# Kernel tuning notes

Hardware: AMD Instinct MI355X
Metric: run time of the kernel (lower is better)

## Reference

```python
import jax, jax.numpy as jnp
import numpy as np

B, W, C, N = 2, 2048, 512, 8
K = C // N                      # 64
HALF = K * (K + 1) // 2 - K     # strict upper-triangle count
EPS = 1e-5


def _layernorm(x, gamma, beta):
    mu = jnp.mean(x, axis=-1, keepdims=True)
    var = jnp.mean(jnp.square(x - mu), axis=-1, keepdims=True)
    return (x - mu) * jax.lax.rsqrt(var + EPS) * gamma + beta


def _build_metric(halves, diagonals):
    # symmetric per-head metric: strict upper triangle from `halves`,
    # mirrored, diagonal overwritten by `diagonals` (diag of m+m^T is 0).
    iu0, iu1 = np.triu_indices(K, k=1)
    m = jnp.zeros((N, K, K), dtype=halves.dtype).at[:, iu0, iu1].set(halves)
    m = m + jnp.swapaxes(m, -1, -2)
    d = np.arange(K)
    return m.at[:, d, d].set(diagonals)


def setup_inputs() -> dict:
    key = jax.random.key(0)
    ks = jax.random.split(key, 9)
    return {
        "x1": jax.random.normal(ks[0], (B, W, C), jnp.float32),
        "x2": jax.random.normal(ks[1], (B, W, C), jnp.float32),
        "gamma": jnp.ones((C,), jnp.float32),
        "beta": jnp.zeros((C,), jnp.float32),
        "proj_nck": jax.random.normal(ks[2], (N, C, K), jnp.float32) * (C ** -0.5),
        "halves": jax.random.normal(ks[3], (N, HALF), jnp.float32) * 0.05,
        "diagonals": jax.random.normal(ks[4], (N, K), jnp.float32) * 0.05,
        "W_mixer": jax.random.normal(ks[5], (C, C), jnp.float32) * 0.02,
        "b_mixer": jnp.zeros((C,), jnp.float32),
    }


def reference(x1, x2, gamma, beta, proj_nck, halves, diagonals, W_mixer, b_mixer):
    x1n = _layernorm(x1, gamma, beta)
    x2n = _layernorm(x2, gamma, beta)
    metric_nkk = _build_metric(halves, diagonals)

    # per-head projections (same projection used for both sequences)
    p1_bnwk = jnp.einsum("bwc,nck->bnwk", x1n, proj_nck)
    p2_bnwk = jnp.einsum("bwc,nck->bnwk", x2n, proj_nck)

    # bilinear metric scores  Q . M . K^T  -> [B, N, W, W]
    dots_bnww = jnp.einsum("bnwk,nkj,bnvj->bnwv", p1_bnwk, metric_nkk, p2_bnwk)

    # NOTE: the original computes a scaled/masked softmax of dots_bnww but
    # never uses it for the output; the value mix uses the RAW dot products.
    # We omit the dead softmax — output math is identical.

    nudged_bnwk = jnp.einsum("bnwv,bnvk->bnwk", dots_bnww, p1_bnwk)
    nudged_bwc = jnp.transpose(nudged_bnwk, (0, 2, 1, 3)).reshape(x1.shape[0], x1.shape[1], C)
    return nudged_bwc @ W_mixer.T + b_mixer
```

## Files before the change

### kernel.cpp

```cpp
#include <hip/hip_runtime.h>

typedef unsigned short u16;
typedef __attribute__((ext_vector_type(8))) short short8;
typedef __attribute__((ext_vector_type(4))) float f32x4;

#define HALFN 2016

__device__ __forceinline__ u16 f2b_rn(float x) {
    union { float f; unsigned u; } v; v.f = x;
    unsigned r = v.u + 0x7FFFu + ((v.u >> 16) & 1u);
    return (u16)(r >> 16);
}

__device__ __forceinline__ void gll16(const void* g, void* s) {
    __builtin_amdgcn_global_load_lds(
        (const __attribute__((address_space(1))) unsigned int*)g,
        (__attribute__((address_space(3))) unsigned int*)s, 16, 0, 0);
}

__global__ __launch_bounds__(256) void ln_prep(const float* __restrict__ x1,
                                               const float* __restrict__ x2,
                                               const float* __restrict__ gamma,
                                               const float* __restrict__ beta,
                                               const float* __restrict__ proj,
                                               u16* __restrict__ Xh,
                                               u16* __restrict__ Pwh,
                                               float* __restrict__ S) {
    __shared__ float ls[8], lq[8];
    __shared__ float tile[64][65];
    const int bid = blockIdx.x, t = threadIdx.x;

    if (bid < 8192) {
        const float* src = (bid < 4096) ? (x1 + (size_t)bid * 512)
                                        : (x2 + (size_t)(bid - 4096) * 512);
        float2 v = *(const float2*)&src[t * 2];
        float s  = v.x + v.y;
        float sq = v.x * v.x + v.y * v.y;
        #pragma unroll
        for (int off = 32; off > 0; off >>= 1) {
            s  += __shfl_down(s, off);
            sq += __shfl_down(sq, off);
        }
        int wave = t >> 6, lane = t & 63;
        if (lane == 0) { ls[wave] = s; lq[wave] = sq; }
        __syncthreads();
        if (t == 0) {
            float Sm = 0.f, Q = 0.f;
            #pragma unroll
            for (int i = 0; i < 4; i++) { Sm += ls[i]; Q += lq[i]; }
            float mu  = Sm * (1.0f / 512.0f);
            float var = Q * (1.0f / 512.0f) - mu * mu;
            ls[4] = mu;
            lq[4] = rsqrtf(var + 1e-5f);
        }
        __syncthreads();
        float mu = ls[4], rs = lq[4];
        float2 g  = *(const float2*)&gamma[t * 2];
        float2 bb = *(const float2*)&beta[t * 2];
        float o0 = (v.x - mu) * rs * g.x + bb.x;
        float o1 = (v.y - mu) * rs * g.y + bb.y;
        ushort2 H; H.x = f2b_rn(o0); H.y = f2b_rn(o1);
        *(ushort2*)&Xh[(size_t)bid * 512 + t * 2] = H;
    } else if (bid < 8256) {
        const int id = bid - 8192;
        const int n = id >> 3, c0 = (id & 7) * 64;
        #pragma unroll
        for (int i = 0; i < 4; i++) {
            int flat = i * 256 + t;
            int c = flat >> 4, k4 = (flat & 15) * 4;
            float4 v = *(const float4*)&proj[(size_t)n * 32768 + (size_t)(c0 + c) * 64 + k4];
            tile[c][k4 + 0] = v.x; tile[c][k4 + 1] = v.y;
            tile[c][k4 + 2] = v.z; tile[c][k4 + 3] = v.w;
        }
        __syncthreads();
        #pragma unroll
        for (int i = 0; i < 16; i++) {
            int flat = i * 256 + t;
            int k = flat >> 6, c = flat & 63;
            Pwh[(size_t)(n * 64 + k) * 512 + c0 + c] = f2b_rn(tile[c][k]);
        }
    } else {
        float4 z = {0.f, 0.f, 0.f, 0.f};
        #pragma unroll
        for (int i = 0; i < 64; i++)
            *(float4*)&S[(size_t)(i * 256 + t) * 4] = z;
    }
}

template<int TM, int TN>
__device__ __forceinline__ void gemm_core_a1b1(const u16* __restrict__ A,
                                               const u16* __restrict__ B,
                                               int m0, int n0, u16* lds,
                                               f32x4 (&acc)[TM / 32][TN / 32]) {
    constexpr int MI = TM / 32, NI = TN / 32;
    constexpr int LA = TM * 32;
    const int t = threadIdx.x;
    const int lane = t & 63;
    const int w = t >> 6, wm = w & 1, wn = w >> 1;
    const int fr = lane & 15, q = lane >> 4;

    int aoff[MI], boff[NI];
    #pragma unroll
    for (int i = 0; i < MI; i++) {
        int r = wm * (TM / 2) + i * 16 + fr;
        aoff[i] = r * 32 + ((q ^ ((r >> 1) & 3)) * 8);
    }
    #pragma unroll
    for (int j = 0; j < NI; j++) {
        int r = wn * (TN / 2) + j * 16 + fr;
        boff[j] = r * 32 + ((q ^ ((r >> 1) & 3)) * 8);
    }

    for (int kt = 0; kt < 512; kt += 32) {
        #pragma unroll
        for (int p = 0; p < TM / 64; p++) {
            int o = p * 4096 + t * 16;
            int r = o >> 6;
            int kc = ((o >> 4) & 3) ^ ((r >> 1) & 3);
            gll16(A + (size_t)(m0 + r) * 512 + kt + kc * 8, lds + (o >> 1));
        }
        #pragma unroll
        for (int p = 0; p < TN / 64; p++) {
            int o = p * 4096 + t * 16;
            int r = o >> 6;
            int kc = ((o >> 4) & 3) ^ ((r >> 1) & 3);
            gll16(B + (size_t)(n0 + r) * 512 + kt + kc * 8, lds + LA + (o >> 1));
        }
        __syncthreads();
        short8 af[MI], bf[NI];
        #pragma unroll
        for (int i = 0; i < MI; i++)
            af[i] = *(const short8*)(lds + aoff[i]);
        #pragma unroll
        for (int j = 0; j < NI; j++)
            bf[j] = *(const short8*)(lds + LA + boff[j]);
        #pragma unroll
        for (int i = 0; i < MI; i++)
            #pragma unroll
            for (int j = 0; j < NI; j++)
                acc[i][j] = __builtin_amdgcn_mfma_f32_16x16x32_bf16(af[i], bf[j], acc[i][j], 0, 0, 0);
        __syncthreads();
    }
}

__global__ __launch_bounds__(256) void gemm_proj_mfma(const u16* __restrict__ Xh,
                                                      const u16* __restrict__ Pwh,
                                                      u16* __restrict__ PPh,
                                                      u16* __restrict__ PPT1h,
                                                      u16* __restrict__ PPT2h) {
    __shared__ u16 lds[6144];
    f32x4 acc[4][2] = {};
    const int m0 = blockIdx.x * 128, n0 = blockIdx.y * 64;
    gemm_core_a1b1<128, 64>(Xh, Pwh, m0, n0, lds, acc);
    const int t = threadIdx.x, lane = t & 63, w = t >> 6, wm = w & 1, wn = w >> 1;
    const int fr = lane & 15, q = lane >> 4;
    const int src2 = (m0 >= 4096);
    const int b = (m0 & 4095) >> 11;
    const int v00 = m0 & 2047;
    #pragma unroll
    for (int i = 0; i < 4; i++) {
        int mloc = wm * 64 + i * 16 + q * 4;
        int v = v00 + mloc;
        #pragma unroll
        for (int j = 0; j < 2; j++) {
            int n = n0 + wn * 32 + j * 16 + fr;
            u16 hs[4];
            #pragma unroll
            for (int r = 0; r < 4; r++) hs[r] = f2b_rn(acc[i][j][r]);
            ushort4 hv; hv.x = hs[0]; hv.y = hs[1]; hv.z = hs[2]; hv.w = hs[3];
            if (!src2) {
                #pragma unroll
                for (int r = 0; r < 4; r++)
                    PPh[(size_t)(m0 + mloc + r) * 512 + n] = hs[r];
                *(ushort4*)&PPT1h[((size_t)(b * 512 + n)) * 2048 + v] = hv;
            } else {
                *(ushort4*)&PPT2h[((size_t)(b * 512 + n)) * 2048 + v] = hv;
            }
        }
    }
}

__global__ __launch_bounds__(256) void s_kernel(const u16* __restrict__ PPT2h,
                                                const u16* __restrict__ PPT1h,
                                                float* __restrict__ S) {
    __shared__ u16 lds[4096];
    const int bn = blockIdx.x, b = bn >> 3, n = bn & 7;
    const u16* A = PPT2h + ((size_t)(b * 512 + n * 64)) * 2048;
    const u16* B = PPT1h + ((size_t)(b * 512 + n * 64)) * 2048;
    const int t = threadIdx.x, lane = t & 63, w = t >> 6, wm = w & 1, wn = w >> 1;
    const int fr = lane & 15, q = lane >> 4;

    int aoff[2], boff[2];
    #pragma unroll
    for (int i = 0; i < 2; i++) {
        int r = wm * 32 + i * 16 + fr;
        aoff[i] = r * 32 + ((q ^ ((r >> 1) & 3)) * 8);
    }
    #pragma unroll
    for (int j = 0; j < 2; j++) {
        int r = wn * 32 + j * 16 + fr;
        boff[j] = r * 32 + ((q ^ ((r >> 1) & 3)) * 8);
    }
    const int o = t * 16;
    const int rr = o >> 6;
    const int kc = ((o >> 4) & 3) ^ ((rr >> 1) & 3);
    const int le = o >> 1;

    f32x4 acc[2][2] = {};
    const int k0 = blockIdx.y * 128;
    for (int kt = k0; kt < k0 + 128; kt += 32) {
        size_t g = (size_t)rr * 2048 + kt + kc * 8;
        gll16(A + g, lds + le);
        gll16(B + g, lds + 2048 + le);
        __syncthreads();
        short8 af[2], bf[2];
        #pragma unroll
        for (int i = 0; i < 2; i++) af[i] = *(const short8*)(lds + aoff[i]);
        #pragma unroll
        for (int j = 0; j < 2; j++) bf[j] = *(const short8*)(lds + 2048 + boff[j]);
        #pragma unroll
        for (int i = 0; i < 2; i++)
            #pragma unroll
            for (int j = 0; j < 2; j++)
                acc[i][j] = __builtin_amdgcn_mfma_f32_16x16x32_bf16(af[i], bf[j], acc[i][j], 0, 0, 0);
        __syncthreads();
    }
    float* Sb = S + (size_t)bn * 4096;
    #pragma unroll
    for (int i = 0; i < 2; i++) {
        int jrow = wm * 32 + i * 16 + q * 4;
        #pragma unroll
        for (int j = 0; j < 2; j++) {
            int kk = wn * 32 + j * 16 + fr;
            #pragma unroll
            for (int r = 0; r < 4; r++)
                atomicAdd(&Sb[(jrow + r) * 64 + kk], acc[i][j][r]);
        }
    }
}

__global__ __launch_bounds__(256) void tu_kernel(const float* __restrict__ S,
                                                 const float* __restrict__ halves,
                                                 const float* __restrict__ diagonals,
                                                 const float* __restrict__ Wm,
                                                 u16* __restrict__ UTh) {
    __shared__ float Ms[64][65];
    __shared__ float Gs[64][68];
    __shared__ float Ts[64][68];
    const int bid = blockIdx.x, t = threadIdx.x;
    const int bn = bid >> 3, b = bn >> 3, n = bn & 7, cy = bid & 7;

    for (int idx = t; idx < 4096; idx += 256) {
        int r = idx >> 6, c = idx & 63;
        float val;
        if (r == c) {
            val = diagonals[n * 64 + r];
        } else {
            int rr = (r < c) ? r : c;
            int cc = (r < c) ? c : r;
            int h = rr * 63 - (rr * (rr - 1)) / 2 + (cc - rr - 1);
            val = halves[n * HALFN + h];
        }
        Ms[r][c] = val;
    }
    for (int idx = t; idx < 4096; idx += 256)
        Gs[idx >> 6][idx & 63] = S[(size_t)bn * 4096 + idx];
    __syncthreads();

    {
        const int k = t & 63, lq = t >> 6;
        float a[16] = {};
        for (int j = 0; j < 64; j++) {
            float m = Ms[k][j];
            const float* gp = &Gs[j][lq * 16];
            #pragma unroll
            for (int u4 = 0; u4 < 4; u4++) {
                float4 g4 = *(const float4*)&gp[u4 * 4];
                a[u4 * 4 + 0] = fmaf(m, g4.x, a[u4 * 4 + 0]);
                a[u4 * 4 + 1] = fmaf(m, g4.y, a[u4 * 4 + 1]);
                a[u4 * 4 + 2] = fmaf(m, g4.z, a[u4 * 4 + 2]);
                a[u4 * 4 + 3] = fmaf(m, g4.w, a[u4 * 4 + 3]);
            }
        }
        int pos = (lq ^ (k & 3)) * 16;
        #pragma unroll
        for (int u4 = 0; u4 < 4; u4++) {
            float4 v4 = {a[u4 * 4 + 0], a[u4 * 4 + 1], a[u4 * 4 + 2], a[u4 * 4 + 3]};
            *(float4*)&Ts[k][pos + u4 * 4] = v4;
        }
    }
    __syncthreads();

    const int k2 = t & 63, cgp = t >> 6;
    const int c0 = cy * 64 + cgp * 16;
    float uacc[16] = {};
    #pragma unroll
    for (int kkc = 0; kkc < 4; kkc++) {
        const float* tp = &Ts[k2][(kkc ^ (k2 & 3)) * 16];
        float ts[16];
        #pragma unroll
        for (int u = 0; u < 4; u++) {
            float4 t4 = *(const float4*)&tp[u * 4];
            ts[u * 4 + 0] = t4.x; ts[u * 4 + 1] = t4.y;
            ts[u * 4 + 2] = t4.z; ts[u * 4 + 3] = t4.w;
        }
        #pragma unroll
        for (int i = 0; i < 16; i++) {
            const float* wrow = &Wm[(size_t)(c0 + i) * 512 + n * 64 + kkc * 16];
            #pragma unroll
            for (int u = 0; u < 4; u++) {
                float4 w4 = *(const float4*)&wrow[u * 4];
                uacc[i] = fmaf(ts[u * 4 + 0], w4.x, uacc[i]);
                uacc[i] = fmaf(ts[u * 4 + 1], w4.y, uacc[i]);
                uacc[i] = fmaf(ts[u * 4 + 2], w4.z, uacc[i]);
                uacc[i] = fmaf(ts[u * 4 + 3], w4.w, uacc[i]);
            }
        }
    }
    #pragma unroll
    for (int i = 0; i < 16; i++)
        UTh[(size_t)b * 262144 + (size_t)(c0 + i) * 512 + n * 64 + k2] = f2b_rn(uacc[i]);
}

__global__ __launch_bounds__(256) void gemm_out_mfma(const u16* __restrict__ PPh,
                                                     const u16* __restrict__ UTh,
                                                     const float* __restrict__ bias,
                                                     float* __restrict__ out) {
    __shared__ u16 lds[4096];
    const int b = blockIdx.z;
    const u16* A = PPh + (size_t)b * 2048 * 512;
    const u16* B = UTh + (size_t)b * 512 * 512;
    f32x4 acc[2][2] = {};
    const int m0 = blockIdx.x * 64, n0 = blockIdx.y * 64;
    gemm_core_a1b1<64, 64>(A, B, m0, n0, lds, acc);
    const int t = threadIdx.x, lane = t & 63, w = t >> 6, wm = w & 1, wn = w >> 1;
    const int fr = lane & 15, q = lane >> 4;
    #pragma unroll
    for (int i = 0; i < 2; i++) {
        int m = m0 + wm * 32 + i * 16 + q * 4;
        #pragma unroll
        for (int j = 0; j < 2; j++) {
            int n = n0 + wn * 32 + j * 16 + fr;
            float bv = bias[n];
            #pragma unroll
            for (int r = 0; r < 4; r++)
                out[(size_t)(b * 2048 + m + r) * 512 + n] = acc[i][j][r] + bv;
        }
    }
}

extern "C" void kernel_launch(void* const* d_in, const int* in_sizes, int n_in,
                              void* d_out, int out_size, void* d_ws, size_t ws_size,
                              hipStream_t stream) {
    (void)in_sizes; (void)n_in; (void)out_size; (void)ws_size;
    const float* x1        = (const float*)d_in[0];
    const float* x2        = (const float*)d_in[1];
    const float* gamma     = (const float*)d_in[2];
    const float* beta      = (const float*)d_in[3];
    const float* proj      = (const float*)d_in[4];
    const float* halves    = (const float*)d_in[5];
    const float* diagonals = (const float*)d_in[6];
    const float* Wm        = (const float*)d_in[7];
    const float* bmix      = (const float*)d_in[8];
    float* out = (float*)d_out;

    u16* us    = (u16*)d_ws;
    u16* Xh    = us;
    u16* Pwh   = Xh + 4194304;
    u16* PPh   = Pwh + 262144;
    u16* PPT1h = PPh + 2097152;
    u16* PPT2h = PPT1h + 2097152;
    u16* UTh   = PPT2h + 2097152;
    float* S   = (float*)(UTh + 524288);

    ln_prep<<<dim3(8257), 256, 0, stream>>>(x1, x2, gamma, beta, proj, Xh, Pwh, S);
    gemm_proj_mfma<<<dim3(64, 8), 256, 0, stream>>>(Xh, Pwh, PPh, PPT1h, PPT2h);
    s_kernel<<<dim3(16, 16), 256, 0, stream>>>(PPT2h, PPT1h, S);
    tu_kernel<<<dim3(128), 256, 0, stream>>>(S, halves, diagonals, Wm, UTh);
    gemm_out_mfma<<<dim3(32, 8, 2), 256, 0, stream>>>(PPh, UTh, bmix, out);
}
```

Baseline: 127.8 us.

## Use one wave per LayerNorm row and a 64-deep K step in the bf16 GEMMs

The LayerNorm prep now gives each row to one wave: each lane reads float4 pairs and the statistics come from wave shuffles alone. This drops the LDS reduction and two block barriers, and cuts the block count by four. The shared MFMA GEMM core now stages a 64-wide K slice per iteration with an 8-way XOR swizzle, which halves the number of barrier-separated load rounds. The cost is double the LDS per block, which may lower occupancy.

```diff
diff --git a/kernel.cpp b/kernel.cpp
--- a/kernel.cpp
+++ b/kernel.cpp
@@ -26,43 +26,46 @@
                                                u16* __restrict__ Xh,
                                                u16* __restrict__ Pwh,
                                                float* __restrict__ S) {
-    __shared__ float ls[8], lq[8];
-    __shared__ float tile[64][65];
     const int bid = blockIdx.x, t = threadIdx.x;
 
-    if (bid < 8192) {
-        const float* src = (bid < 4096) ? (x1 + (size_t)bid * 512)
-                                        : (x2 + (size_t)(bid - 4096) * 512);
-        float2 v = *(const float2*)&src[t * 2];
-        float s  = v.x + v.y;
-        float sq = v.x * v.x + v.y * v.y;
+    if (bid < 2048) {
+        const int wv = t >> 6, lane = t & 63;
+        const int row = bid * 4 + wv;
+        const float* src = (row < 4096) ? (x1 + (size_t)row * 512)
+                                        : (x2 + (size_t)(row - 4096) * 512);
+        float4 v0 = *(const float4*)&src[lane * 4];
+        float4 v1 = *(const float4*)&src[256 + lane * 4];
+        float s  = v0.x + v0.y + v0.z + v0.w + v1.x + v1.y + v1.z + v1.w;
+        float sq = v0.x * v0.x + v0.y * v0.y + v0.z * v0.z + v0.w * v0.w +
+                   v1.x * v1.x + v1.y * v1.y + v1.z * v1.z + v1.w * v1.w;
         #pragma unroll
         for (int off = 32; off > 0; off >>= 1) {
             s  += __shfl_down(s, off);
             sq += __shfl_down(sq, off);
         }
-        int wave = t >> 6, lane = t & 63;
-        if (lane == 0) { ls[wave] = s; lq[wave] = sq; }
-        __syncthreads();
-        if (t == 0) {
-            float Sm = 0.f, Q = 0.f;
-            #pragma unroll
-            for (int i = 0; i < 4; i++) { Sm += ls[i]; Q += lq[i]; }
-            float mu  = Sm * (1.0f / 512.0f);
-            float var = Q * (1.0f / 512.0f) - mu * mu;
-            ls[4] = mu;
-            lq[4] = rsqrtf(var + 1e-5f);
-        }
-        __syncthreads();
-        float mu = ls[4], rs = lq[4];
-        float2 g  = *(const float2*)&gamma[t * 2];
-        float2 bb = *(const float2*)&beta[t * 2];
-        float o0 = (v.x - mu) * rs * g.x + bb.x;
-        float o1 = (v.y - mu) * rs * g.y + bb.y;
-        ushort2 H; H.x = f2b_rn(o0); H.y = f2b_rn(o1);
-        *(ushort2*)&Xh[(size_t)bid * 512 + t * 2] = H;
-    } else if (bid < 8256) {
-        const int id = bid - 8192;
+        s  = __shfl(s, 0);
+        sq = __shfl(sq, 0);
+        float mu  = s * (1.0f / 512.0f);
+        float var = sq * (1.0f / 512.0f) - mu * mu;
+        float rs  = rsqrtf(var + 1e-5f);
+        float4 g0 = *(const float4*)&gamma[lane * 4];
+        float4 g1 = *(const float4*)&gamma[256 + lane * 4];
+        float4 b0 = *(const float4*)&beta[lane * 4];
+        float4 b1 = *(const float4*)&beta[256 + lane * 4];
+        ushort4 h0, h1;
+        h0.x = f2b_rn((v0.x - mu) * rs * g0.x + b0.x);
+        h0.y = f2b_rn((v0.y - mu) * rs * g0.y + b0.y);
+        h0.z = f2b_rn((v0.z - mu) * rs * g0.z + b0.z);
+        h0.w = f2b_rn((v0.w - mu) * rs * g0.w + b0.w);
+        h1.x = f2b_rn((v1.x - mu) * rs * g1.x + b1.x);
+        h1.y = f2b_rn((v1.y - mu) * rs * g1.y + b1.y);
+        h1.z = f2b_rn((v1.z - mu) * rs * g1.z + b1.z);
+        h1.w = f2b_rn((v1.w - mu) * rs * g1.w + b1.w);
+        *(ushort4*)&Xh[(size_t)row * 512 + lane * 4] = h0;
+        *(ushort4*)&Xh[(size_t)row * 512 + 256 + lane * 4] = h1;
+    } else if (bid < 2112) {
+        __shared__ float tile[64][65];
+        const int id = bid - 2048;
         const int n = id >> 3, c0 = (id & 7) * 64;
         #pragma unroll
         for (int i = 0; i < 4; i++) {
@@ -88,57 +91,63 @@
 }
 
 template<int TM, int TN>
-__device__ __forceinline__ void gemm_core_a1b1(const u16* __restrict__ A,
+__device__ __forceinline__ void gemm_core_bk64(const u16* __restrict__ A,
                                                const u16* __restrict__ B,
-                                               int m0, int n0, u16* lds,
+                                               int m0, int n0, int ld, u16* lds,
                                                f32x4 (&acc)[TM / 32][TN / 32]) {
     constexpr int MI = TM / 32, NI = TN / 32;
-    constexpr int LA = TM * 32;
+    constexpr int LA = TM * 64;
     const int t = threadIdx.x;
     const int lane = t & 63;
     const int w = t >> 6, wm = w & 1, wn = w >> 1;
     const int fr = lane & 15, q = lane >> 4;
 
-    int aoff[MI], boff[NI];
-    #pragma unroll
-    for (int i = 0; i < MI; i++) {
-        int r = wm * (TM / 2) + i * 16 + fr;
-        aoff[i] = r * 32 + ((q ^ ((r >> 1) & 3)) * 8);
-    }
-    #pragma unroll
-    for (int j = 0; j < NI; j++) {
-        int r = wn * (TN / 2) + j * 16 + fr;
-        boff[j] = r * 32 + ((q ^ ((r >> 1) & 3)) * 8);
-    }
-
-    for (int kt = 0; kt < 512; kt += 32) {
-        #pragma unroll
-        for (int p = 0; p < TM / 64; p++) {
+    int aoff[2][MI], boff[2][NI];
+    #pragma unroll
+    for (int kc = 0; kc < 2; kc++) {
+        #pragma unroll
+        for (int i = 0; i < MI; i++) {
+            int r = wm * (TM / 2) + i * 16 + fr;
+            aoff[kc][i] = r * 64 + (((kc * 4 + q) ^ (r & 7)) * 8);
+        }
+        #pragma unroll
+        for (int j = 0; j < NI; j++) {
+            int r = wn * (TN / 2) + j * 16 + fr;
+            boff[kc][j] = r * 64 + (((kc * 4 + q) ^ (r & 7)) * 8);
+        }
+    }
+
+    for (int kt = 0; kt < 512; kt += 64) {
+        #pragma unroll
+        for (int p = 0; p < TM / 32; p++) {
             int o = p * 4096 + t * 16;
-            int r = o >> 6;
-            int kc = ((o >> 4) & 3) ^ ((r >> 1) & 3);
-            gll16(A + (size_t)(m0 + r) * 512 + kt + kc * 8, lds + (o >> 1));
-        }
-        #pragma unroll
-        for (int p = 0; p < TN / 64; p++) {
+            int r = o >> 7;
+            int c = ((o >> 4) & 7) ^ (r & 7);
+            gll16(A + (size_t)(m0 + r) * ld + kt + c * 8, lds + (o >> 1));
+        }
+        #pragma unroll
+        for (int p = 0; p < TN / 32; p++) {
             int o = p * 4096 + t * 16;
-            int r = o >> 6;
-            int kc = ((o >> 4) & 3) ^ ((r >> 1) & 3);
-            gll16(B + (size_t)(n0 + r) * 512 + kt + kc * 8, lds + LA + (o >> 1));
-        }
-        __syncthreads();
-        short8 af[MI], bf[NI];
-        #pragma unroll
-        for (int i = 0; i < MI; i++)
-            af[i] = *(const short8*)(lds + aoff[i]);
-        #pragma unroll
-        for (int j = 0; j < NI; j++)
-            bf[j] = *(const short8*)(lds + LA + boff[j]);
-        #pragma unroll
-        for (int i = 0; i < MI; i++)
+            int r = o >> 7;
+            int c = ((o >> 4) & 7) ^ (r & 7);
+            gll16(B + (size_t)(n0 + r) * ld + kt + c * 8, lds + LA + (o >> 1));
+        }
+        __syncthreads();
+        #pragma unroll
+        for (int kc = 0; kc < 2; kc++) {
+            short8 af[MI], bf[NI];
+            #pragma unroll
+            for (int i = 0; i < MI; i++)
+                af[i] = *(const short8*)(lds + aoff[kc][i]);
             #pragma unroll
             for (int j = 0; j < NI; j++)
-                acc[i][j] = __builtin_amdgcn_mfma_f32_16x16x32_bf16(af[i], bf[j], acc[i][j], 0, 0, 0);
+                bf[j] = *(const short8*)(lds + LA + boff[kc][j]);
+            #pragma unroll
+            for (int i = 0; i < MI; i++)
+                #pragma unroll
+                for (int j = 0; j < NI; j++)
+                    acc[i][j] = __builtin_amdgcn_mfma_f32_16x16x32_bf16(af[i], bf[j], acc[i][j], 0, 0, 0);
+        }
         __syncthreads();
     }
 }
@@ -148,10 +157,10 @@
                                                       u16* __restrict__ PPh,
                                                       u16* __restrict__ PPT1h,
                                                       u16* __restrict__ PPT2h) {
-    __shared__ u16 lds[6144];
+    __shared__ u16 lds[12288];
     f32x4 acc[4][2] = {};
     const int m0 = blockIdx.x * 128, n0 = blockIdx.y * 64;
-    gemm_core_a1b1<128, 64>(Xh, Pwh, m0, n0, lds, acc);
+    gemm_core_bk64<128, 64>(Xh, Pwh, m0, n0, 512, lds, acc);
     const int t = threadIdx.x, lane = t & 63, w = t >> 6, wm = w & 1, wn = w >> 1;
     const int fr = lane & 15, q = lane >> 4;
     const int src2 = (m0 >= 4096);
@@ -326,13 +335,13 @@
                                                      const u16* __restrict__ UTh,
                                                      const float* __restrict__ bias,
                                                      float* __restrict__ out) {
-    __shared__ u16 lds[4096];
+    __shared__ u16 lds[8192];
     const int b = blockIdx.z;
     const u16* A = PPh + (size_t)b * 2048 * 512;
     const u16* B = UTh + (size_t)b * 512 * 512;
     f32x4 acc[2][2] = {};
     const int m0 = blockIdx.x * 64, n0 = blockIdx.y * 64;
-    gemm_core_a1b1<64, 64>(A, B, m0, n0, lds, acc);
+    gemm_core_bk64<64, 64>(A, B, m0, n0, 512, lds, acc);
     const int t = threadIdx.x, lane = t & 63, w = t >> 6, wm = w & 1, wn = w >> 1;
     const int fr = lane & 15, q = lane >> 4;
     #pragma unroll
@@ -373,7 +382,7 @@
     u16* UTh   = PPT2h + 2097152;
     float* S   = (float*)(UTh + 524288);
 
-    ln_prep<<<dim3(8257), 256, 0, stream>>>(x1, x2, gamma, beta, proj, Xh, Pwh, S);
+    ln_prep<<<dim3(2113), 256, 0, stream>>>(x1, x2, gamma, beta, proj, Xh, Pwh, S);
     gemm_proj_mfma<<<dim3(64, 8), 256, 0, stream>>>(Xh, Pwh, PPh, PPT1h, PPT2h);
     s_kernel<<<dim3(16, 16), 256, 0, stream>>>(PPT2h, PPT1h, S);
     tu_kernel<<<dim3(128), 256, 0, stream>>>(S, halves, diagonals, Wm, UTh);
```

New measurement: 124.1 us. 2.9% less time.
